# Performance work log

Measured on AMD Instinct MI355X. Metric: run time of the kernel, lower is better.

The kernel has to match this reference:

```python
import jax, jax.numpy as jnp
import numpy as np

N = 100000      # nodes
E = 3200000     # edges
IN = 64         # in_channels
OUT = 256       # out_channels (hidden)
OSZ = 4         # output_size


def setup_inputs() -> dict:
    key = jax.random.key(0)
    ks = jax.random.split(key, 16)
    s = 0.05
    inp = {
        "x": jax.random.normal(ks[0], (N, IN), jnp.float32),
        "edge_index": jax.random.randint(ks[1], (2, E), 0, N, jnp.int64),
        # GCNConv weights for z, r, h gates: [IN, OUT] + bias [OUT]
        "Wz": jax.random.normal(ks[2], (IN, OUT), jnp.float32) * s,
        "bz": jnp.zeros((OUT,), jnp.float32),
        "Wr": jax.random.normal(ks[3], (IN, OUT), jnp.float32) * s,
        "br": jnp.zeros((OUT,), jnp.float32),
        "Wh": jax.random.normal(ks[4], (IN, OUT), jnp.float32) * s,
        "bh": jnp.zeros((OUT,), jnp.float32),
        # GRU linear layers: [2*OUT, OUT] + bias [OUT]
        "Lzw": jax.random.normal(ks[5], (2 * OUT, OUT), jnp.float32) * s,
        "Lzb": jnp.zeros((OUT,), jnp.float32),
        "Lrw": jax.random.normal(ks[6], (2 * OUT, OUT), jnp.float32) * s,
        "Lrb": jnp.zeros((OUT,), jnp.float32),
        "Lhw": jax.random.normal(ks[7], (2 * OUT, OUT), jnp.float32) * s,
        "Lhb": jnp.zeros((OUT,), jnp.float32),
        # output head
        "Wo": jax.random.normal(ks[8], (OUT, OSZ), jnp.float32) * s,
        "bo": jnp.zeros((OSZ,), jnp.float32),
    }
    return inp


def _gcn_conv(x, W, b, src, dst, n):
    # GCNConv with symmetric normalization and self-loops (fill_value=1):
    # out = D^{-1/2}(A+I)D^{-1/2} X W + b
    ones = jnp.ones_like(src, dtype=x.dtype)
    deg = jax.ops.segment_sum(ones, dst, num_segments=n) + 1.0  # +1 for self-loop
    dinv = jax.lax.rsqrt(deg)                                   # [N]
    norm = dinv[src] * dinv[dst]                                # [E]
    agg = jax.ops.segment_sum(x[src] * norm[:, None], dst, num_segments=n)
    agg = agg + x * (dinv * dinv)[:, None]                      # self-loop term
    return agg @ W + b


def reference(x, edge_index, Wz, bz, Wr, br, Wh, bh,
              Lzw, Lzb, Lrw, Lrb, Lhw, Lhb, Wo, bo):
    src, dst = edge_index[0], edge_index[1]
    n = x.shape[0]
    H = jnp.zeros((n, Wz.shape[1]), x.dtype)  # TGCN initial hidden state
    # update gate
    Z = jax.nn.sigmoid(jnp.concatenate([_gcn_conv(x, Wz, bz, src, dst, n), H], 1) @ Lzw + Lzb)
    # reset gate
    R = jax.nn.sigmoid(jnp.concatenate([_gcn_conv(x, Wr, br, src, dst, n), H], 1) @ Lrw + Lrb)
    # candidate state
    Ht = jnp.tanh(jnp.concatenate([_gcn_conv(x, Wh, bh, src, dst, n), H * R], 1) @ Lhw + Lhb)
    H = Z * H + (1.0 - Z) * Ht
    # head: ReLU -> Linear -> Softmax(dim=1)
    h = jax.nn.relu(H)
    return jax.nn.softmax(h @ Wo + bo, axis=1)
```

## Files before the change

### kernel.cpp

```cpp
#include <hip/hip_runtime.h>
#include <hip/hip_fp16.h>


#define SHIFT 7
#define NPB   128
#define BMAX  1024
#define TILE  8192
#define EPT   16
#define CAPB  5120

typedef __attribute__((ext_vector_type(8))) short short8;
typedef __attribute__((ext_vector_type(4))) float floatx4;

__device__ __forceinline__ ushort f2b(float f) {
    union { float f; unsigned u; } v; v.f = f;
    unsigned r = v.u + 0x7FFFu + ((v.u >> 16) & 1u);
    return (ushort)(r >> 16);
}

__device__ __forceinline__ float fastrcp(float x) {
    return __builtin_amdgcn_rcpf(x);
}

__global__ __launch_bounds__(512) void scatter_kernel(
    const int* __restrict__ srcs, const int* __restrict__ dsts,
    int* __restrict__ gcur, int* __restrict__ staging, int E, int B) {
    __shared__ int cnt[BMAX];
    __shared__ int ssum[BMAX];
    __shared__ int gbase[BMAX];
    __shared__ int cur[BMAX];
    __shared__ int sorted[TILE];
    int tid = threadIdx.x;
    for (int i = tid; i < BMAX; i += 512) cnt[i] = 0;
    __syncthreads();
    int tile0 = blockIdx.x * TILE;
    int dreg[EPT];
#pragma unroll
    for (int j = 0; j < EPT; ++j) {
        int e = tile0 + j * 512 + tid;
        dreg[j] = (e < E) ? dsts[e] : -1;
        if (dreg[j] >= 0) atomicAdd(&cnt[((unsigned)dreg[j]) >> SHIFT], 1);
    }
    __syncthreads();
    {
        int i0 = tid, i1 = tid + 512;
        ssum[i0] = cnt[i0];
        ssum[i1] = cnt[i1];
        __syncthreads();
        for (int off = 1; off < BMAX; off <<= 1) {
            int t0 = (i0 >= off) ? ssum[i0 - off] : 0;
            int t1 = (i1 >= off) ? ssum[i1 - off] : 0;
            __syncthreads();
            ssum[i0] += t0;
            ssum[i1] += t1;
            __syncthreads();
        }
    }
    for (int i = tid; i < BMAX; i += 512) {
        int c = cnt[i];
        gbase[i] = (c > 0) ? atomicAdd(&gcur[i], c) : 0;
        cur[i] = ssum[i] - c;
    }
    __syncthreads();
#pragma unroll
    for (int j = 0; j < EPT; ++j) {
        int d = dreg[j];
        if (d >= 0) {
            int e = tile0 + j * 512 + tid;
            int s = srcs[e];
            int b = ((unsigned)d) >> SHIFT;
            int pos = atomicAdd(&cur[b], 1);
            sorted[pos] = ((d & (NPB - 1)) << 17) | s;
        }
    }
    __syncthreads();
    int grp = tid >> 4, l16 = tid & 15;
    for (int b = grp; b < B; b += 32) {
        int c = cnt[b];
        if (c == 0) continue;
        int lb = ssum[b] - c;
        int gb = gbase[b];
        size_t gp = (size_t)b * CAPB + gb;
        for (int j = l16; j < c; j += 16)
            if (gb + j < CAPB) staging[gp + j] = sorted[lb + j];
    }
}

__global__ __launch_bounds__(512) void build_m_kernel(
    const float* __restrict__ Wz, const float* __restrict__ bz,
    const float* __restrict__ Wh, const float* __restrict__ bh,
    const float* __restrict__ Lzw, const float* __restrict__ Lzb,
    const float* __restrict__ Lhw, const float* __restrict__ Lhb,
    ushort* __restrict__ Mb, float* __restrict__ cb) {
    int j = blockIdx.x * 8 + (threadIdx.x >> 6);
    int k = threadIdx.x & 63;
    int which = j >> 8;
    int jj = j & 255;
    const float* W  = which ? Wh  : Wz;
    const float* bv = which ? bh  : bz;
    const float* L  = which ? Lhw : Lzw;
    const float* Lb = which ? Lhb : Lzb;
    const float4* Wr = (const float4*)(W + k * 256);
    float acc = 0.f;
    for (int t4 = 0; t4 < 64; ++t4) {
        float4 wv = Wr[t4];
        int t = t4 * 4;
        acc = fmaf(wv.x, L[(t + 0) * 256 + jj], acc);
        acc = fmaf(wv.y, L[(t + 1) * 256 + jj], acc);
        acc = fmaf(wv.z, L[(t + 2) * 256 + jj], acc);
        acc = fmaf(wv.w, L[(t + 3) * 256 + jj], acc);
    }
    Mb[j * 64 + k] = f2b(acc);
    if (k == 0) {
        float a = 0.f;
        for (int t = 0; t < 256; ++t) a = fmaf(bv[t], L[t * 256 + jj], a);
        cb[j] = a + Lb[jj];
    }
}

__global__ __launch_bounds__(512) void prep_kernel(const int* __restrict__ staging,
                                                   const int* __restrict__ gcur,
                                                   const float* __restrict__ x,
                                                   int* __restrict__ deg,
                                                   __half* __restrict__ xs,
                                                   int n, int B) {
    int b = blockIdx.x;
    int tid = threadIdx.x;
    __shared__ int nd[NPB];
    __shared__ float sdinv[NPB];
    if (tid < NPB) nd[tid] = 0;
    __syncthreads();
    int count = gcur[b];
    if (count > CAPB) count = CAPB;
    size_t base = (size_t)b * CAPB;
    for (int i = tid; i < count; i += 512)
        atomicAdd(&nd[staging[base + i] >> 17], 1);
    __syncthreads();
    if (tid < NPB) {
        int dg = nd[tid];
        float dn = rsqrtf((float)dg + 1.0f);
        sdinv[tid] = dn;
        int node = (b << SHIFT) + tid;
        if (node < n) deg[node] = dg;
    }
    __syncthreads();
    int nbase = b << SHIFT;
    for (int i2 = tid; i2 < NPB * 16; i2 += 512) {
        int nl = i2 >> 4;
        int node = nbase + nl;
        if (node < n) {
            float dn = sdinv[nl];
            size_t gi = (size_t)node * 16 + (i2 & 15);
            float4 vx = ((const float4*)x)[gi];
            __half2 a = __floats2half2_rn(vx.x * dn, vx.y * dn);
            __half2 c = __floats2half2_rn(vx.z * dn, vx.w * dn);
            ((__half2*)xs)[gi * 2 + 0] = a;
            ((__half2*)xs)[gi * 2 + 1] = c;
        }
    }
}

__global__ __launch_bounds__(512) void bucket_gather_kernel(
    const int* __restrict__ staging,
    const int* __restrict__ gcur,
    const int* __restrict__ deg,
    const __half* __restrict__ xs,
    ushort* __restrict__ aggb, int n, int B, int par) {
    int b   = (blockIdx.x << 1) | par;
    if (b >= B) return;
    int tid = threadIdx.x;
    __shared__ int   csrl[CAPB];
    __shared__ int   sstart[NPB];
    __shared__ int   ncur[NPB];
    __shared__ int   sdeg[NPB];
    __shared__ int   ssc[NPB];
    __shared__ float sdinv[NPB];
    int node0 = b << SHIFT;
    int count = gcur[b];
    if (count > CAPB) count = CAPB;
    size_t base = (size_t)b * CAPB;
    if (tid < NPB) {
        int nodeid = node0 + tid;
        int dg = (nodeid < n) ? deg[nodeid] : 0;
        sdeg[tid] = dg;
        ssc[tid]  = dg;
        sdinv[tid] = rsqrtf((float)dg + 1.0f);
    }
    __syncthreads();
    for (int off = 1; off < NPB; off <<= 1) {
        int t = 0;
        if (tid < NPB && tid >= off) t = ssc[tid - off];
        __syncthreads();
        if (tid < NPB) ssc[tid] += t;
        __syncthreads();
    }
    if (tid < NPB) {
        int excl = ssc[tid] - sdeg[tid];
        sstart[tid] = excl;
        ncur[tid]   = excl;
    }
    __syncthreads();
    for (int i = tid; i < count; i += 512) {
        int p = staging[base + i];
        int pos = atomicAdd(&ncur[p >> 17], 1);
        if (pos < CAPB) csrl[pos] = p & 0x1FFFF;
    }
    __syncthreads();
    int wv = tid >> 6, lane = tid & 63;
    int eg = lane >> 3;
    int c  = lane & 7;
    for (int t16 = 0; t16 < 16; ++t16) {
        int nl   = (wv << 4) + t16;
        int node = node0 + nl;
        int s0 = sstart[nl];
        int d  = sdeg[nl];
        __half2 hz = __float2half2_rn(0.f);
        __half2 hacc[4] = {hz, hz, hz, hz};
        int full = d & ~15;
        for (int be = 0; be < full; be += 16) {
            int qb = s0 + be;
            if (qb > CAPB - 16) qb = CAPB - 16;
            int i0 = csrl[qb + eg];
            int i1 = csrl[qb + 8 + eg];
            union { uint4 u; __half2 h[4]; } p0, p1;
            p0.u = *(const uint4*)(xs + (size_t)i0 * 64 + c * 8);
            p1.u = *(const uint4*)(xs + (size_t)i1 * 64 + c * 8);
#pragma unroll
            for (int t = 0; t < 4; ++t) hacc[t] = __hadd2(hacc[t], p0.h[t]);
#pragma unroll
            for (int t = 0; t < 4; ++t) hacc[t] = __hadd2(hacc[t], p1.h[t]);
        }
        if (full < d) {
            int e0 = full + eg;
            int e1 = full + 8 + eg;
            int q0 = s0 + (e0 < d ? e0 : d - 1);
            int q1 = s0 + (e1 < d ? e1 : d - 1);
            if (q0 > CAPB - 1) q0 = CAPB - 1;
            if (q1 > CAPB - 1) q1 = CAPB - 1;
            int i0 = csrl[q0];
            int i1 = csrl[q1];
            union { uint4 u; __half2 h[4]; } p0, p1;
            p0.u = *(const uint4*)(xs + (size_t)i0 * 64 + c * 8);
            p1.u = *(const uint4*)(xs + (size_t)i1 * 64 + c * 8);
            if (e0 >= d) p0.u = make_uint4(0u, 0u, 0u, 0u);
            if (e1 >= d) p1.u = make_uint4(0u, 0u, 0u, 0u);
#pragma unroll
            for (int t = 0; t < 4; ++t) hacc[t] = __hadd2(hacc[t], p0.h[t]);
#pragma unroll
            for (int t = 0; t < 4; ++t) hacc[t] = __hadd2(hacc[t], p1.h[t]);
        }
#pragma unroll
        for (int off = 32; off >= 8; off >>= 1) {
#pragma unroll
            for (int t = 0; t < 4; ++t) {
                union { __half2 h; int i; } u;
                u.h = hacc[t];
                u.i = __shfl_down(u.i, off);
                hacc[t] = __hadd2(hacc[t], u.h);
            }
        }
        if (eg == 0 && node < n) {
            float dn = sdinv[nl];
            union { uint4 u; __half2 h[4]; } p;
            p.u = *(const uint4*)(xs + (size_t)node * 64 + c * 8);
            uint4 o;
            unsigned* ow = (unsigned*)&o;
#pragma unroll
            for (int t = 0; t < 4; ++t) {
                float2 a = __half22float2(hacc[t]);
                float2 f = __half22float2(p.h[t]);
                float v0 = dn * fmaf(f.x, dn, a.x);
                float v1 = dn * fmaf(f.y, dn, a.y);
                ow[t] = (unsigned)f2b(v0) | ((unsigned)f2b(v1) << 16);
            }
            ((uint4*)(aggb + (size_t)node * 64))[c] = o;
        }
    }
}

__global__ __launch_bounds__(512) void node_mfma_kernel(
    const ushort* __restrict__ aggb,
    const ushort* __restrict__ Mb,
    const float* __restrict__ cb,
    const float* __restrict__ Wo, const float* __restrict__ bo,
    float* __restrict__ out, int n) {
    int tid  = threadIdx.x;
    int w    = tid >> 6;
    int lane = tid & 63;
    int nidx = lane & 15;
    int quad = lane >> 4;
    short8 bfz[2][2], bfh[2][2];
    float cbz[2], cbh[2];
#pragma unroll
    for (int cg = 0; cg < 2; ++cg) {
        int colZ = (w << 5) + (cg << 4) + nidx;
        int colH = 256 + colZ;
#pragma unroll
        for (int s = 0; s < 2; ++s) {
            bfz[cg][s] = *(const short8*)(Mb + colZ * 64 + s * 32 + quad * 8);
            bfh[cg][s] = *(const short8*)(Mb + colH * 64 + s * 32 + quad * 8);
        }
        cbz[cg] = cb[colZ];
        cbh[cg] = cb[colH];
    }
    __shared__ float sH[32][260];
    __shared__ float sWo[4][256];
    if (tid < 256) {
#pragma unroll
        for (int o = 0; o < 4; ++o) sWo[o][tid] = Wo[tid * 4 + o];
    }
    float bo0 = bo[0], bo1 = bo[1], bo2 = bo[2], bo3 = bo[3];
    int ntiles = (n + 31) >> 5;
    for (int tile = blockIdx.x; tile < ntiles; tile += gridDim.x) {
        int node0 = tile << 5;
        int nA0 = node0 + nidx;
        int nA1 = node0 + 16 + nidx;
        if (nA0 >= n) nA0 = n - 1;
        if (nA1 >= n) nA1 = n - 1;
        const ushort* ar0 = aggb + (size_t)nA0 * 64;
        const ushort* ar1 = aggb + (size_t)nA1 * 64;
        short8 a00 = *(const short8*)(ar0 + quad * 8);
        short8 a01 = *(const short8*)(ar0 + 32 + quad * 8);
        short8 a10 = *(const short8*)(ar1 + quad * 8);
        short8 a11 = *(const short8*)(ar1 + 32 + quad * 8);
#pragma unroll
        for (int cg = 0; cg < 2; ++cg) {
            int col = (w << 5) + (cg << 4) + nidx;
#pragma unroll
            for (int grp = 0; grp < 2; ++grp) {
                short8 a0 = grp ? a10 : a00;
                short8 a1 = grp ? a11 : a01;
                floatx4 cz = {cbz[cg], cbz[cg], cbz[cg], cbz[cg]};
                cz = __builtin_amdgcn_mfma_f32_16x16x32_bf16(a0, bfz[cg][0], cz, 0, 0, 0);
                cz = __builtin_amdgcn_mfma_f32_16x16x32_bf16(a1, bfz[cg][1], cz, 0, 0, 0);
                floatx4 chh = {cbh[cg], cbh[cg], cbh[cg], cbh[cg]};
                chh = __builtin_amdgcn_mfma_f32_16x16x32_bf16(a0, bfh[cg][0], chh, 0, 0, 0);
                chh = __builtin_amdgcn_mfma_f32_16x16x32_bf16(a1, bfh[cg][1], chh, 0, 0, 0);
#pragma unroll
                for (int r = 0; r < 4; ++r) {
                    int row = (grp << 4) + (quad << 2) + r;
                    float zc = fastrcp(1.0f + __expf(cz[r]));
                    float th = 1.0f - 2.0f * fastrcp(1.0f + __expf(2.0f * chh[r]));
                    sH[row][col] = fmaxf(zc * th, 0.0f);
                }
            }
        }
        __syncthreads();
        {
            int nb = tid >> 4, g = tid & 15;
            float l0 = 0.f, l1 = 0.f, l2 = 0.f, l3 = 0.f;
#pragma unroll
            for (int ii = 0; ii < 16; ++ii) {
                int ch = g + 16 * ii;
                float hv = sH[nb][ch];
                l0 = fmaf(hv, sWo[0][ch], l0);
                l1 = fmaf(hv, sWo[1][ch], l1);
                l2 = fmaf(hv, sWo[2][ch], l2);
                l3 = fmaf(hv, sWo[3][ch], l3);
            }
#pragma unroll
            for (int off = 8; off > 0; off >>= 1) {
                l0 += __shfl_down(l0, off, 16);
                l1 += __shfl_down(l1, off, 16);
                l2 += __shfl_down(l2, off, 16);
                l3 += __shfl_down(l3, off, 16);
            }
            int node = node0 + nb;
            if (g == 0 && node < n) {
                float v0 = l0 + bo0, v1 = l1 + bo1, v2 = l2 + bo2, v3 = l3 + bo3;
                float mx = fmaxf(fmaxf(v0, v1), fmaxf(v2, v3));
                float e0 = __expf(v0 - mx), e1 = __expf(v1 - mx);
                float e2 = __expf(v2 - mx), e3 = __expf(v3 - mx);
                float inv = fastrcp(e0 + e1 + e2 + e3);
                float4 o;
                o.x = e0 * inv; o.y = e1 * inv; o.z = e2 * inv; o.w = e3 * inv;
                ((float4*)out)[node] = o;
            }
        }
        __syncthreads();
    }
}

extern "C" void kernel_launch(void* const* d_in, const int* in_sizes, int n_in,
                              void* d_out, int out_size, void* d_ws, size_t ws_size,
                              hipStream_t stream) {
    const float* x   = (const float*)d_in[0];
    const int*  eidx = (const int*)d_in[1];
    const float* Wz  = (const float*)d_in[2];
    const float* bz  = (const float*)d_in[3];
    const float* Wh  = (const float*)d_in[6];
    const float* bh  = (const float*)d_in[7];
    const float* Lzw = (const float*)d_in[8];
    const float* Lzb = (const float*)d_in[9];
    const float* Lhw = (const float*)d_in[12];
    const float* Lhb = (const float*)d_in[13];
    const float* Wo  = (const float*)d_in[14];
    const float* bo  = (const float*)d_in[15];
    float* out = (float*)d_out;

    int n = in_sizes[0] / 64;
    int E = in_sizes[1] / 2;
    const int* srcs = eidx;
    const int* dsts = eidx + E;
    int B = (n + NPB - 1) >> SHIFT;
    int nT = (E + TILE - 1) / TILE;

    size_t na = ((size_t)n + 3) & ~(size_t)3;
    size_t stageBytes = (((size_t)B * CAPB * 4) + 255) & ~(size_t)255;
    size_t aggBytes   = (((size_t)n * 64 * 2) + 255) & ~(size_t)255;

    char* ws = (char*)d_ws;
    int*   deg   = (int*)ws;    ws += na * 4;
    int*   gcur  = (int*)ws;    ws += BMAX * 4;
    int*   staging = (int*)ws;  ws += stageBytes;
    __half* xs   = (__half*)ws; ws += (size_t)n * 64 * 2;
    ushort* aggb = (ushort*)ws; ws += aggBytes;
    ushort* Mb   = (ushort*)ws; ws += 512 * 64 * 2;
    float* cb    = (float*)ws;  ws += 512 * 4;

    hipMemsetAsync(gcur, 0, BMAX * 4, stream);
    scatter_kernel<<<nT, 512, 0, stream>>>(srcs, dsts, gcur, staging, E, B);
    build_m_kernel<<<64, 512, 0, stream>>>(Wz, bz, Wh, bh,
                                           Lzw, Lzb, Lhw, Lhb, Mb, cb);
    prep_kernel<<<B, 512, 0, stream>>>(staging, gcur, x, deg, xs, n, B);
    int Bh0 = (B + 1) >> 1;
    int Bh1 = B >> 1;
    bucket_gather_kernel<<<Bh0, 512, 0, stream>>>(staging, gcur, deg,
                                                  xs, aggb, n, B, 0);
    bucket_gather_kernel<<<Bh1, 512, 0, stream>>>(staging, gcur, deg,
                                                  xs, aggb, n, B, 1);
    node_mfma_kernel<<<1024, 512, 0, stream>>>(aggb, Mb, cb, Wo, bo, out, n);
}
```

Before: 276.7 us.

## Move per-bucket prefix scan into prep kernel and merge gather launches

The per-bucket exclusive prefix scan of node degrees now runs in prep_kernel, which writes per-node start offsets to a new global array. bucket_gather_kernel reads those offsets instead of redoing the barrier-heavy scan. The two parity-split gather launches become a single launch over all buckets. Staging reads in both kernels are vectorised to int4. This trades an extra small global write and read for fewer syncthreads and one fewer launch, and the int4 loads assume the staging base is 16-byte aligned.

```diff
diff --git a/kernel.cpp b/kernel.cpp
--- a/kernel.cpp
+++ b/kernel.cpp
@@ -122,26 +122,50 @@
                                                    const int* __restrict__ gcur,
                                                    const float* __restrict__ x,
                                                    int* __restrict__ deg,
+                                                   int* __restrict__ startg,
                                                    __half* __restrict__ xs,
                                                    int n, int B) {
     int b = blockIdx.x;
     int tid = threadIdx.x;
     __shared__ int nd[NPB];
+    __shared__ int ssc[NPB];
     __shared__ float sdinv[NPB];
     if (tid < NPB) nd[tid] = 0;
     __syncthreads();
     int count = gcur[b];
     if (count > CAPB) count = CAPB;
     size_t base = (size_t)b * CAPB;
-    for (int i = tid; i < count; i += 512)
+    const int4* w4 = (const int4*)(staging + base);
+    int n4 = count >> 2;
+    for (int i = tid; i < n4; i += 512) {
+        int4 p = w4[i];
+        atomicAdd(&nd[p.x >> 17], 1);
+        atomicAdd(&nd[p.y >> 17], 1);
+        atomicAdd(&nd[p.z >> 17], 1);
+        atomicAdd(&nd[p.w >> 17], 1);
+    }
+    for (int i = (n4 << 2) + tid; i < count; i += 512)
         atomicAdd(&nd[staging[base + i] >> 17], 1);
     __syncthreads();
+    int d0 = 0;
+    if (tid < NPB) { d0 = nd[tid]; ssc[tid] = d0; }
+    __syncthreads();
+    for (int off = 1; off < NPB; off <<= 1) {
+        int t = 0;
+        if (tid < NPB && tid >= off) t = ssc[tid - off];
+        __syncthreads();
+        if (tid < NPB) ssc[tid] += t;
+        __syncthreads();
+    }
     if (tid < NPB) {
-        int dg = nd[tid];
+        int dg = d0;
         float dn = rsqrtf((float)dg + 1.0f);
         sdinv[tid] = dn;
         int node = (b << SHIFT) + tid;
-        if (node < n) deg[node] = dg;
+        if (node < n) {
+            deg[node] = dg;
+            startg[node] = ssc[tid] - dg;
+        }
     }
     __syncthreads();
     int nbase = b << SHIFT;
@@ -164,16 +188,15 @@
     const int* __restrict__ staging,
     const int* __restrict__ gcur,
     const int* __restrict__ deg,
+    const int* __restrict__ startg,
     const __half* __restrict__ xs,
-    ushort* __restrict__ aggb, int n, int B, int par) {
-    int b   = (blockIdx.x << 1) | par;
-    if (b >= B) return;
+    ushort* __restrict__ aggb, int n, int B) {
+    int b   = blockIdx.x;
     int tid = threadIdx.x;
     __shared__ int   csrl[CAPB];
     __shared__ int   sstart[NPB];
     __shared__ int   ncur[NPB];
     __shared__ int   sdeg[NPB];
-    __shared__ int   ssc[NPB];
     __shared__ float sdinv[NPB];
     int node0 = b << SHIFT;
     int count = gcur[b];
@@ -182,28 +205,29 @@
     if (tid < NPB) {
         int nodeid = node0 + tid;
         int dg = (nodeid < n) ? deg[nodeid] : 0;
-        sdeg[tid] = dg;
-        ssc[tid]  = dg;
-        sdinv[tid] = rsqrtf((float)dg + 1.0f);
-    }
-    __syncthreads();
-    for (int off = 1; off < NPB; off <<= 1) {
-        int t = 0;
-        if (tid < NPB && tid >= off) t = ssc[tid - off];
-        __syncthreads();
-        if (tid < NPB) ssc[tid] += t;
-        __syncthreads();
-    }
-    if (tid < NPB) {
-        int excl = ssc[tid] - sdeg[tid];
-        sstart[tid] = excl;
-        ncur[tid]   = excl;
-    }
-    __syncthreads();
-    for (int i = tid; i < count; i += 512) {
-        int p = staging[base + i];
-        int pos = atomicAdd(&ncur[p >> 17], 1);
-        if (pos < CAPB) csrl[pos] = p & 0x1FFFF;
+        int st = (nodeid < n) ? startg[nodeid] : 0;
+        sdeg[tid]   = dg;
+        sstart[tid] = st;
+        ncur[tid]   = st;
+        sdinv[tid]  = rsqrtf((float)dg + 1.0f);
+    }
+    __syncthreads();
+    {
+        const int4* w4 = (const int4*)(staging + base);
+        int n4 = count >> 2;
+        for (int i = tid; i < n4; i += 512) {
+            int4 p = w4[i];
+            int pos;
+            pos = atomicAdd(&ncur[p.x >> 17], 1); if (pos < CAPB) csrl[pos] = p.x & 0x1FFFF;
+            pos = atomicAdd(&ncur[p.y >> 17], 1); if (pos < CAPB) csrl[pos] = p.y & 0x1FFFF;
+            pos = atomicAdd(&ncur[p.z >> 17], 1); if (pos < CAPB) csrl[pos] = p.z & 0x1FFFF;
+            pos = atomicAdd(&ncur[p.w >> 17], 1); if (pos < CAPB) csrl[pos] = p.w & 0x1FFFF;
+        }
+        for (int i = (n4 << 2) + tid; i < count; i += 512) {
+            int p = staging[base + i];
+            int pos = atomicAdd(&ncur[p >> 17], 1);
+            if (pos < CAPB) csrl[pos] = p & 0x1FFFF;
+        }
     }
     __syncthreads();
     int wv = tid >> 6, lane = tid & 63;
@@ -410,8 +434,9 @@
     size_t aggBytes   = (((size_t)n * 64 * 2) + 255) & ~(size_t)255;
 
     char* ws = (char*)d_ws;
-    int*   deg   = (int*)ws;    ws += na * 4;
-    int*   gcur  = (int*)ws;    ws += BMAX * 4;
+    int*   deg    = (int*)ws;   ws += na * 4;
+    int*   startg = (int*)ws;   ws += na * 4;
+    int*   gcur   = (int*)ws;   ws += BMAX * 4;
     int*   staging = (int*)ws;  ws += stageBytes;
     __half* xs   = (__half*)ws; ws += (size_t)n * 64 * 2;
     ushort* aggb = (ushort*)ws; ws += aggBytes;
@@ -422,12 +447,8 @@
     scatter_kernel<<<nT, 512, 0, stream>>>(srcs, dsts, gcur, staging, E, B);
     build_m_kernel<<<64, 512, 0, stream>>>(Wz, bz, Wh, bh,
                                            Lzw, Lzb, Lhw, Lhb, Mb, cb);
-    prep_kernel<<<B, 512, 0, stream>>>(staging, gcur, x, deg, xs, n, B);
-    int Bh0 = (B + 1) >> 1;
-    int Bh1 = B >> 1;
-    bucket_gather_kernel<<<Bh0, 512, 0, stream>>>(staging, gcur, deg,
-                                                  xs, aggb, n, B, 0);
-    bucket_gather_kernel<<<Bh1, 512, 0, stream>>>(staging, gcur, deg,
-                                                  xs, aggb, n, B, 1);
+    prep_kernel<<<B, 512, 0, stream>>>(staging, gcur, x, deg, startg, xs, n, B);
+    bucket_gather_kernel<<<B, 512, 0, stream>>>(staging, gcur, deg, startg,
+                                                xs, aggb, n, B);
     node_mfma_kernel<<<1024, 512, 0, stream>>>(aggb, Mb, cb, Wo, bo, out, n);
 }
```

Measured after the change: 258.1 us. -6.7%, faster.
